# Kernel tuning notes

Hardware: AMD Instinct MI355X
Metric: run time of the kernel (lower is better)

Reference implementation:

```python
import jax, jax.numpy as jnp
import numpy as np

B, IN, CB, HD, EXP, OUT, FC1 = 512, 512, 8, 256, 128, 512, 1024
CH = CB * HD            # 2048, combiner output channels
CC = IN + CH            # 2560, concat feature size
EPS = 1e-5

def _lrelu(x):
    return jnp.where(x >= 0, x, 0.2 * x)

def _bn2(x, g, b):  # BatchNorm1d on (B, C): stats over batch
    m = x.mean(0)
    v = x.var(0)
    return (x - m) * jax.lax.rsqrt(v + EPS) * g + b

def _bn3(x, g, b):  # BatchNorm1d/2d on (B, C, L): stats over (batch, length)
    m = x.mean((0, 2), keepdims=True)
    v = x.var((0, 2), keepdims=True)
    return (x - m) * jax.lax.rsqrt(v + EPS) * g[None, :, None] + b[None, :, None]

def _cmix(W, x):  # 1x1 conv over channels: (O,I) x (B,I,L) -> (B,O,L)
    return jnp.einsum('oi,bil->bol', W, x)

def setup_inputs() -> dict:
    key = jax.random.key(0)
    ks = jax.random.split(key, 16)
    def w(k, o, i):
        return jax.random.normal(k, (o, i), jnp.float32) * (1.0 / np.sqrt(i))
    u = jax.random.uniform(ks[1], (B, CB, HD, 1), jnp.float32, 1e-6, 1.0 - 1e-6)
    return {
        'x': jax.random.normal(ks[0], (B, IN), jnp.float32),
        'gumbel': -jnp.log(-jnp.log(u)),
        # combiner (Linear no-bias + BN + LeakyReLU) x3
        'cW1': w(ks[2], 2 * IN, IN), 'cg1': jnp.ones(2 * IN), 'cb1': jnp.zeros(2 * IN),
        'cW2': w(ks[3], 2 * IN, 2 * IN), 'cg2': jnp.ones(2 * IN), 'cb2': jnp.zeros(2 * IN),
        'cW3': w(ks[4], CH, 2 * IN), 'cg3': jnp.ones(CH), 'cb3': jnp.zeros(CH),
        # encoder Conv2d1x1 stack 1 -> 32 -> 64 -> 128
        'eW1': w(ks[5], EXP // 4, 1), 'eg1': jnp.ones(EXP // 4), 'eb1': jnp.zeros(EXP // 4),
        'eW2': w(ks[6], EXP // 2, EXP // 4), 'eg2': jnp.ones(EXP // 2), 'eb2': jnp.zeros(EXP // 2),
        'eW3': w(ks[7], EXP, EXP // 2), 'eg3': jnp.ones(EXP), 'eb3': jnp.zeros(EXP),
        # fc Conv1d1x1: 2560 -> 1024 (BN+lrelu), 1024 -> OUT (bias, no act)
        'fW1': w(ks[8], FC1, CC), 'fg1': jnp.ones(FC1), 'fb1': jnp.zeros(FC1),
        'fW2': w(ks[9], OUT, FC1), 'fbias2': jnp.zeros(OUT),
        # decoder Conv1d1x1: 128 -> 64 -> 32 -> 1
        'dW1': w(ks[10], EXP // 2, EXP), 'dg1': jnp.ones(EXP // 2), 'db1': jnp.zeros(EXP // 2),
        'dW2': w(ks[11], EXP // 4, EXP // 2), 'dg2': jnp.ones(EXP // 4), 'db2': jnp.zeros(EXP // 4),
        'dW3': w(ks[12], 1, EXP // 4), 'dbias3': jnp.zeros(1),
    }

def _forward(x, gumbel, cW1, cg1, cb1, cW2, cg2, cb2, cW3, cg3, cb3,
             eW1, eg1, eb1, eW2, eg2, eb2, eW3, eg3, eb3,
             fW1, fg1, fb1, fW2, fbias2,
             dW1, dg1, db1, dW2, dg2, db2, dW3, dbias3):
    # ---- combiner: logits for gumbel-softmax hard codebook selection ----
    h = _lrelu(_bn2(x @ cW1.T, cg1, cb1))
    h = _lrelu(_bn2(h @ cW2.T, cg2, cb2))
    logits = _lrelu(_bn2(h @ cW3.T, cg3, cb3)).reshape(B, CB, HD, 1)
    y = jax.nn.softmax(logits + gumbel, axis=1)  # tau = 1 (torch default)
    hard = jax.nn.one_hot(jnp.argmax(y, axis=1), CB, axis=1, dtype=y.dtype)
    w = (hard - jax.lax.stop_gradient(y) + y)[..., 0]  # (B, CB, HD) straight-through
    # weight last dim is size-1, so broadcast-mul + sum(-1) against x collapses
    # exactly to w * sum_j x_j (same math, no (B,CB,HD,IN) intermediate).
    S = x.sum(-1)          # (B,)
    S2 = (x * x).sum(-1)   # (B,)
    xs = (w * S[:, None, None]).reshape(B, CH)
    xp = (w * S2[:, None, None]).reshape(B, CH)
    z = (xs * xs - xp) * 0.5
    feat = jnp.concatenate([x, z], axis=-1)  # (B, CC)
    # ---- encoder: Conv2d1x1 stack on (B,1,1,CC) == channel mix over length CC ----
    t = feat[:, None, :]  # (B, 1, CC)
    t = _lrelu(_bn3(_cmix(eW1, t), eg1, eb1))
    t = _lrelu(_bn3(_cmix(eW2, t), eg2, eb2))
    t = _lrelu(_bn3(_cmix(eW3, t), eg3, eb3))  # (B, EXP, CC)
    # ---- fc: Conv1d over channels=CC, length=EXP ----
    t = jnp.swapaxes(t, 1, 2)  # (B, CC, EXP)
    t = _lrelu(_bn3(_cmix(fW1, t), fg1, fb1))          # (B, FC1, EXP)
    t = _cmix(fW2, t) + fbias2[None, :, None]          # (B, OUT, EXP)
    # ---- decoder: Conv1d over channels=EXP, length=OUT ----
    t = jnp.swapaxes(t, 1, 2)  # (B, EXP, OUT)
    t = _lrelu(_bn3(_cmix(dW1, t), dg1, db1))
    t = _lrelu(_bn3(_cmix(dW2, t), dg2, db2))
    t = _cmix(dW3, t) + dbias3[None, :, None]  # (B, 1, OUT)
    return t[:, 0, :]  # (B, OUT)

def reference(x, gumbel, cW1, cg1, cb1, cW2, cg2, cb2, cW3, cg3, cb3,
              eW1, eg1, eb1, eW2, eg2, eb2, eW3, eg3, eb3,
              fW1, fg1, fb1, fW2, fbias2,
              dW1, dg1, db1, dW2, dg2, db2, dW3, dbias3):
    return _forward(x, gumbel, cW1, cg1, cb1, cW2, cg2, cb2, cW3, cg3, cb3,
                    eW1, eg1, eb1, eW2, eg2, eb2, eW3, eg3, eb3,
                    fW1, fg1, fb1, fW2, fbias2,
                    dW1, dg1, db1, dW2, dg2, db2, dW3, dbias3)
```

## Files before the change

kernel.cpp:

```cpp
#include <hip/hip_runtime.h>
#include <cstddef>

#define DEV __device__ __forceinline__
DEV float lrelu(float x){ return x >= 0.0f ? x : 0.2f*x; }
typedef _Float16 f16;
typedef _Float16 f16x8 __attribute__((ext_vector_type(8)));
typedef float f32x4 __attribute__((ext_vector_type(4)));

DEV f16x8 splat8(f16 s){ f16x8 v = {s,s,s,s,s,s,s,s}; return v; }
DEV f16x8 bnl8(f16x8 v, f16x8 sc, f16x8 sh){
    f16x8 t = v*sc + sh;
    f16x8 z = splat8((f16)0.0f);
    f16x8 mx = __builtin_elementwise_max(t, z);
    f16x8 mn = __builtin_elementwise_min(t, z);
    return mx + mn*splat8((f16)0.2f);
}

DEV void gload_lds16(const f16* src, f16* dst){
    __builtin_amdgcn_global_load_lds(
        (const __attribute__((address_space(1))) void*)src,
        (__attribute__((address_space(3))) void*)dst, 16, 0, 0);
}

DEV void dma_pair(const f16* g0, const f16* g1, f16* ldsbase, int t){
    gload_lds16(g0, ldsbase + t*8);
    gload_lds16(g1, ldsbase + 2048 + t*8);
}
DEV int swz_off(int r, int g){ return r*32 + ((g ^ ((r>>1)&3))<<3); }

#define SCHED0 __builtin_amdgcn_sched_barrier(0)
#define BARRIER __builtin_amdgcn_s_barrier()

constexpr int NXPT = 512*512;

constexpr size_t O_H1  = 0;
constexpr size_t O_H2  = O_H1 + 512*1024;
constexpr size_t O_L   = O_H2 + 512*1024;
constexpr size_t O_SEL = O_L  + 512*2048;
constexpr size_t O_S   = O_SEL + 512*256;
constexpr size_t O_S2  = O_S + 512;
constexpr size_t O_VAL = O_S2 + 512;
constexpr size_t O_PRM = O_VAL + 512;
constexpr size_t P_SC1=0, P_SH1=1024, P_SC2=2048, P_SH2=3072, P_SC3=4096, P_SH3=6144;
constexpr size_t P_A1=8192, P_C1=8224, P_EW2T=8256 ;
constexpr size_t P_ACC2=18496 , P_ACC3=18624 ;
constexpr size_t P_SCE2=18880, P_SHE2=18944, P_SCE3=19008, P_SHE3=19136;
constexpr size_t P_U0=19264 , P_FTOT=19392 ;
constexpr size_t P_SCF1=20416, P_SHF1=21440;
constexpr size_t P_SCD1=22464, P_SHD1=22528, P_SCD2=22592, P_SHD2=22624;
constexpr size_t P_SCE3H=22656, P_SHE3H=22720;
constexpr size_t P_SCF1H=22784, P_SHF1H=23296;
constexpr size_t P_SCE2H=23808, P_SHE2H=23840;
constexpr size_t PRM_SIZE = 32768;
constexpr size_t O_PF  = O_H1;
constexpr size_t O_PD1 = O_H2;
constexpr size_t O_PD2 = O_H2 + 262144;
constexpr size_t O_FW1H = O_L;
constexpr size_t O_FW2H = O_L + 262144;
constexpr size_t O_ACCF = O_L + 524288;
constexpr size_t O_DW1H = O_L + 528384;
constexpr size_t O_EW3H = O_L + 532480;
constexpr size_t O_V2SS = O_L + 536576;
constexpr size_t O_U1  = O_PRM + PRM_SIZE;
constexpr size_t O_P1  = O_U1 + 512*128;
constexpr size_t O_FZT = O_P1 + 512*1024;
constexpr size_t O_V3S = O_FZT + (size_t)2048*1024;
constexpr size_t O_BIG1= O_V3S + 513*128;
constexpr size_t O_BIG2= O_BIG1 + (size_t)512*512*128/2;
constexpr size_t O_D1  = O_BIG2;
constexpr size_t O_D2  = O_BIG2 + (size_t)512*64*512;
constexpr size_t O_END = O_BIG2 + (size_t)512*1024*128/2;

#define FMA44(av,bv) do{ \
  acc[0][0]=fmaf(av.x,bv.x,acc[0][0]); acc[0][1]=fmaf(av.x,bv.y,acc[0][1]); \
  acc[0][2]=fmaf(av.x,bv.z,acc[0][2]); acc[0][3]=fmaf(av.x,bv.w,acc[0][3]); \
  acc[1][0]=fmaf(av.y,bv.x,acc[1][0]); acc[1][1]=fmaf(av.y,bv.y,acc[1][1]); \
  acc[1][2]=fmaf(av.y,bv.z,acc[1][2]); acc[1][3]=fmaf(av.y,bv.w,acc[1][3]); \
  acc[2][0]=fmaf(av.z,bv.x,acc[2][0]); acc[2][1]=fmaf(av.z,bv.y,acc[2][1]); \
  acc[2][2]=fmaf(av.z,bv.z,acc[2][2]); acc[2][3]=fmaf(av.z,bv.w,acc[2][3]); \
  acc[3][0]=fmaf(av.w,bv.x,acc[3][0]); acc[3][1]=fmaf(av.w,bv.y,acc[3][1]); \
  acc[3][2]=fmaf(av.w,bv.z,acc[3][2]); acc[3][3]=fmaf(av.w,bv.w,acc[3][3]); \
}while(0)

__global__ void k_sentinel(float* out){ out[blockIdx.x*256 + threadIdx.x] = 1.0e6f; }

__global__ __launch_bounds__(256) void k_prep(
    const float* __restrict__ fW1, const float* __restrict__ fW2,
    const float* __restrict__ dW1, const float* __restrict__ eW3,
    f16* __restrict__ fW1h, f16* __restrict__ fW2h, f16* __restrict__ dW1h,
    f16* __restrict__ eW3h, float* __restrict__ accAll)
{
    const int i = blockIdx.x*256 + threadIdx.x;
    int f = i >> 9, l = i & 511;
    fW1h[i] = (f16)fW1[(size_t)f*2560 + l];
    fW2h[i] = (f16)fW2[i];
    if (i < 8192) { dW1h[i] = (f16)dW1[i]; eW3h[i] = (f16)eW3[i]; }
    if (i < 4096) accAll[i] = 0.f;
}

__global__ __launch_bounds__(256) void k_gemm_c(
    const float* __restrict__ A, const float* __restrict__ W, float* __restrict__ C,
    int N, int K, const float* __restrict__ sc, const float* __restrict__ sh)
{
    __shared__ __align__(16) float As[16][68];
    __shared__ __align__(16) float Ws[16][68];
    const int n0 = blockIdx.x * 64, m0 = blockIdx.y * 64;
    const int t = threadIdx.x;
    const int kk = t & 15, ri = t >> 4;
    const int tx = t & 15, ty = t >> 4;
    float acc[4][4] = {{0.f,0.f,0.f,0.f},{0.f,0.f,0.f,0.f},{0.f,0.f,0.f,0.f},{0.f,0.f,0.f,0.f}};
    for (int k0 = 0; k0 < K; k0 += 16) {
        float scv = 0.f, shv = 0.f;
        if (sc) { scv = sc[k0+kk]; shv = sh[k0+kk]; }
        #pragma unroll
        for (int mm = 0; mm < 4; ++mm) {
            float v = A[(size_t)(m0 + ri + mm*16) * K + k0 + kk];
            if (sc) v = lrelu(fmaf(v, scv, shv));
            As[kk][ri + mm*16] = v;
        }
        #pragma unroll
        for (int nn = 0; nn < 4; ++nn)
            Ws[kk][ri + nn*16] = W[(size_t)(n0 + ri + nn*16) * K + k0 + kk];
        __syncthreads();
        #pragma unroll
        for (int kq = 0; kq < 16; ++kq) {
            const float4 av = *reinterpret_cast<const float4*>(&As[kq][ty*4]);
            const float4 bv = *reinterpret_cast<const float4*>(&Ws[kq][tx*4]);
            FMA44(av, bv);
        }
        __syncthreads();
    }
    #pragma unroll
    for (int i = 0; i < 4; ++i)
        #pragma unroll
        for (int j = 0; j < 4; ++j)
            C[(size_t)(m0 + ty*4 + i) * N + n0 + tx*4 + j] = acc[i][j];
}

__global__ __launch_bounds__(256) void k_stats2d_p(
    const float* __restrict__ buf, int C, float* __restrict__ part)
{
    const int t = threadIdx.x;
    const int r0 = blockIdx.x*16;
    const int c0 = blockIdx.y*1024;
    float s[4]={0.f,0.f,0.f,0.f}, s2[4]={0.f,0.f,0.f,0.f};
    for (int rr = 0; rr < 16; ++rr) {
        float4 v = *reinterpret_cast<const float4*>(buf + (size_t)(r0+rr)*C + c0 + t*4);
        s[0]+=v.x; s[1]+=v.y; s[2]+=v.z; s[3]+=v.w;
        s2[0]+=v.x*v.x; s2[1]+=v.y*v.y; s2[2]+=v.z*v.z; s2[3]+=v.w*v.w;
    }
    float* d0 = part + (size_t)blockIdx.x*2*C + c0 + t*4;
    *reinterpret_cast<float4*>(d0)     = (float4){s[0],s[1],s[2],s[3]};
    *reinterpret_cast<float4*>(d0 + C) = (float4){s2[0],s2[1],s2[2],s2[3]};
}

__global__ __launch_bounds__(256) void k_sel(
    const float* __restrict__ Lpre, const float* __restrict__ gumbel,
    const float* __restrict__ sc, const float* __restrict__ sh, int* __restrict__ sel)
{
    const int b = blockIdx.x, hd = threadIdx.x;
    float best = -3.0e38f; int bi = 0;
    #pragma unroll
    for (int cb = 0; cb < 8; ++cb) {
        int c = cb*256 + hd;
        float v = lrelu(fmaf(Lpre[(size_t)b*2048 + c], sc[c], sh[c])) + gumbel[(size_t)b*2048 + c];
        if (v > best) { best = v; bi = cb; }
    }
    sel[b*256 + hd] = bi;
}

__global__ __launch_bounds__(256) void k_val(const float* __restrict__ x,
    float* __restrict__ S, float* __restrict__ S2, float* __restrict__ val)
{
    const int b = blockIdx.x, t = threadIdx.x;
    float v0 = x[b*512 + t], v1 = x[b*512 + t + 256];
    __shared__ float ls[256], ls2[256];
    ls[t] = v0 + v1; ls2[t] = v0*v0 + v1*v1;
    __syncthreads();
    for (int off = 128; off; off >>= 1) { if (t < off) { ls[t]+=ls[t+off]; ls2[t]+=ls2[t+off]; } __syncthreads(); }
    if (t == 0) { float s = ls[0], s2 = ls2[0]; S[b]=s; S2[b]=s2; val[b]=0.5f*(s*s - s2); }
}

__global__ __launch_bounds__(256) void k_e1params(
    const float* __restrict__ S, const float* __restrict__ S2, const float* __restrict__ val,
    const float* __restrict__ eW1, const float* __restrict__ eg1, const float* __restrict__ eb1,
    float* __restrict__ A1, float* __restrict__ C1, float* __restrict__ accs )
{
    const int t = threadIdx.x;
    accs[t] = 0.f; if (t < 128) accs[256 + t] = 0.f;
    __shared__ float ls[256], ls2[256];
    float s = 0.f, s2 = 0.f;
    for (int b = t; b < 512; b += 256) {
        float vb = val[b];
        s  += S[b]  + 256.f*vb;
        s2 += S2[b] + 256.f*vb*vb;
    }
    ls[t] = s; ls2[t] = s2; __syncthreads();
    for (int off = 128; off; off >>= 1) { if (t < off) { ls[t]+=ls[t+off]; ls2[t]+=ls2[t+off]; } __syncthreads(); }
    if (t < 32) {
        const float invn = 1.0f/1310720.f;
        float mu = ls[0]*invn;
        float var = fmaxf(ls2[0]*invn - mu*mu, 0.f);
        float w = eW1[t];
        float rs = 1.0f / sqrtf(w*w*var + 1e-5f);
        float a = w * eg1[t] * rs;
        A1[t] = a; C1[t] = eb1[t] - mu*a;
    }
}

__global__ void k_wtrans2(const float* __restrict__ eW2, float* __restrict__ eW2T)
{
    const int t = threadIdx.x;
    for (int i = t; i < 2048; i += 256) { int p = i >> 5, o = i & 31; eW2T[o*64 + p] = eW2[i]; }
}

__global__ __launch_bounds__(256) void k_transpose_fz(const float* __restrict__ fW1, float* __restrict__ fzT)
{
    __shared__ float tile[64][65];
    const int z0 = blockIdx.x*64, f0 = blockIdx.y*64;
    const int j = threadIdx.x & 63, i0 = threadIdx.x >> 6;
    #pragma unroll
    for (int ii = 0; ii < 16; ++ii) {
        int fi = i0*16 + ii;
        tile[fi][j] = fW1[(size_t)(f0+fi)*2560 + 512 + z0 + j];
    }
    __syncthreads();
    #pragma unroll
    for (int ii = 0; ii < 16; ++ii) {
        int zi = i0*16 + ii;
        fzT[(size_t)(z0+zi)*1024 + f0 + j] = tile[j][zi];
    }
}

__global__ __launch_bounds__(256) void k_ftot(const float* __restrict__ fzT, float* __restrict__ Ftot)
{
    const int f = blockIdx.x*256 + threadIdx.x;
    float s = 0.f;
    for (int z = 0; z < 2048; ++z) s += fzT[(size_t)z*1024 + f];
    Ftot[f] = s;
}

__global__ __launch_bounds__(256) void k_p1(const float* __restrict__ fzT, const int* __restrict__ sel,
                                            float* __restrict__ P1)
{
    const int b = blockIdx.x, t = threadIdx.x;
    float a0=0.f, a1=0.f, a2=0.f, a3=0.f;
    for (int hd = 0; hd < 256; ++hd) {
        int col = sel[b*256 + hd]*256 + hd;
        const float* r = fzT + (size_t)col*1024;
        a0 += r[t]; a1 += r[t+256]; a2 += r[t+512]; a3 += r[t+768];
    }
    P1[b*1024 + t] = a0; P1[b*1024 + t + 256] = a1; P1[b*1024 + t + 512] = a2; P1[b*1024 + t + 768] = a3;
}

__global__ __launch_bounds__(256) void k_epass2(
    const float* __restrict__ x,
    const float* __restrict__ A1, const float* __restrict__ C1,
    const float* __restrict__ eW2T, f16* __restrict__ V2x)
{
    __shared__ float sW[2048], sA[32], sC[32];
    const int t = threadIdx.x;
    #pragma unroll
    for (int i = 0; i < 8; ++i) sW[t + 256*i] = eW2T[t + 256*i];
    if (t < 32) { sA[t] = A1[t]; sC[t] = C1[t]; }
    __syncthreads();
    const int pt = blockIdx.x*256 + t;
    float phi = x[pt];
    float v2[64];
    #pragma unroll
    for (int p = 0; p < 64; ++p) v2[p] = 0.f;
    for (int o = 0; o < 32; ++o) {
        float t1 = lrelu(fmaf(sA[o], phi, sC[o]));
        #pragma unroll
        for (int p = 0; p < 64; ++p) v2[p] = fmaf(sW[o*64 + p], t1, v2[p]);
    }
    f16* dst = V2x + (size_t)pt*64;
    #pragma unroll
    for (int dd = 0; dd < 64; dd += 8) {
        f16x8 o;
        #pragma unroll
        for (int e = 0; e < 8; ++e) o[e] = (f16)v2[dd+e];
        *reinterpret_cast<f16x8*>(dst + dd) = o;
    }
}

__global__ __launch_bounds__(64) void k_esupport2(
    const float* __restrict__ val,
    const float* __restrict__ A1, const float* __restrict__ C1,
    const float* __restrict__ eW2T, float* __restrict__ V2s)
{
    const int idx = blockIdx.x, d = threadIdx.x;
    float phi = (idx < 512) ? val[idx] : 0.f;
    __shared__ float t1s[32];
    if (d < 32) t1s[d] = lrelu(fmaf(A1[d], phi, C1[d]));
    __syncthreads();
    float s = 0.f;
    #pragma unroll
    for (int o = 0; o < 32; ++o) s = fmaf(eW2T[o*64 + d], t1s[o], s);
    V2s[idx*64 + d] = s;
}

__global__ __launch_bounds__(64) void k_wstats(
    const float* __restrict__ V, int C, float* __restrict__ acc)
{
    const int c = blockIdx.x, lane = threadIdx.x;
    float s = 0.f, s2 = 0.f;
    for (int i = lane; i < 513; i += 64) {
        float w = (i < 512) ? 256.f : 917504.f;
        float v = V[(size_t)i*C + c];
        s += w*v; s2 += w*v*v;
    }
    #pragma unroll
    for (int off = 32; off; off >>= 1) { s += __shfl_xor(s, off); s2 += __shfl_xor(s2, off); }
    if (lane == 0) { atomicAdd(&acc[c], s); atomicAdd(&acc[C + c], s2); }
}

__global__ __launch_bounds__(256) void k_stats_v2scan(const f16* __restrict__ V2x, float* __restrict__ acc2)
{
    const int t = threadIdx.x;
    const int wave = t >> 6, lane = t & 63;
    const int g = t & 7;
    const int slot = blockIdx.x*32 + (t >> 3);
    float s[8] = {0,0,0,0,0,0,0,0}, s2[8] = {0,0,0,0,0,0,0,0};
    for (int p = slot; p < NXPT; p += 2048) {
        f16x8 v = *reinterpret_cast<const f16x8*>(V2x + (size_t)p*64 + g*8);
        #pragma unroll
        for (int e = 0; e < 8; ++e) { float f = (float)v[e]; s[e] += f; s2[e] += f*f; }
    }
    #pragma unroll
    for (int off = 8; off <= 32; off <<= 1) {
        #pragma unroll
        for (int e = 0; e < 8; ++e) { s[e] += __shfl_xor(s[e], off); s2[e] += __shfl_xor(s2[e], off); }
    }
    __shared__ float red[4*128];
    if (lane < 8) {
        #pragma unroll
        for (int e = 0; e < 8; ++e) {
            red[wave*128 + lane*16 + e]     = s[e];
            red[wave*128 + lane*16 + 8 + e] = s2[e];
        }
    }
    __syncthreads();
    if (t < 128) {
        float v = red[t] + red[128 + t] + red[256 + t] + red[384 + t];
        int gg = t >> 4, k = t & 15;
        if (k < 8) atomicAdd(&acc2[gg*8 + k], v);
        else       atomicAdd(&acc2[64 + gg*8 + (k - 8)], v);
    }
}

__global__ void k_finalize(const float* __restrict__ acc, int C, float invn,
                           const float* __restrict__ g, const float* __restrict__ bb,
                           float* __restrict__ sc, float* __restrict__ sh,
                           f16* __restrict__ sch, f16* __restrict__ shh)
{
    const int idx = blockIdx.x*blockDim.x + threadIdx.x;
    if (idx < C) {
        float m = acc[idx] * invn;
        float var = fmaxf(acc[C + idx] * invn - m*m, 0.f);
        float r = 1.0f / sqrtf(var + 1e-5f);
        float s = g[idx] * r;
        float h = bb[idx] - m*s;
        sc[idx] = s; sh[idx] = h;
        if (sch) { sch[idx] = (f16)s; shh[idx] = (f16)h; }
    }
}

__global__ void k_finalize_p(const float* __restrict__ P, int C, int nPart, float invn,
                             const float* __restrict__ g, const float* __restrict__ bb,
                             float* __restrict__ sc, float* __restrict__ sh,
                             f16* __restrict__ sch, f16* __restrict__ shh)
{
    const int idx = blockIdx.x*blockDim.x + threadIdx.x;
    if (idx < C) {
        float s = 0.f, s2 = 0.f;
        for (int p = 0; p < nPart; ++p) {
            s  += P[(size_t)p*2*C + idx];
            s2 += P[(size_t)p*2*C + C + idx];
        }
        float m = s * invn;
        float var = fmaxf(s2 * invn - m*m, 0.f);
        float r = 1.0f / sqrtf(var + 1e-5f);
        float sv = g[idx] * r;
        float h = bb[idx] - m*sv;
        sc[idx] = sv; sh[idx] = h;
        if (sch) { sch[idx] = (f16)sv; shh[idx] = (f16)h; }
    }
}

__global__ __launch_bounds__(256) void k_finalize_e3(
    const float* __restrict__ P, const float* __restrict__ accw,
    const float* __restrict__ g, const float* __restrict__ bb,
    float* __restrict__ sc, float* __restrict__ sh,
    f16* __restrict__ sch, f16* __restrict__ shh)
{
    const int t = threadIdx.x, q = t & 127, h = t >> 7;
    float s = 0.f, s2 = 0.f;
    for (int p = h*1024; p < h*1024 + 1024; ++p) {
        s  += P[(size_t)p*256 + q];
        s2 += P[(size_t)p*256 + 128 + q];
    }
    __shared__ float red[2][2][128];
    red[h][0][q] = s; red[h][1][q] = s2;
    __syncthreads();
    if (t < 128) {
        float ss  = red[0][0][q] + red[1][0][q] + accw[q];
        float ss2 = red[0][1][q] + red[1][1][q] + accw[128 + q];
        const float invn = 1.0f/1310720.f;
        float m = ss * invn;
        float var = fmaxf(ss2 * invn - m*m, 0.f);
        float r = 1.0f / sqrtf(var + 1e-5f);
        float sv = g[q] * r, hh = bb[q] - m*sv;
        sc[q] = sv; sh[q] = hh; sch[q] = (f16)sv; shh[q] = (f16)hh;
    }
}

__global__ __launch_bounds__(256) void k_finalize_f(
    const float* __restrict__ P,
    const float* __restrict__ g, const float* __restrict__ bb,
    float* __restrict__ sc, float* __restrict__ sh,
    f16* __restrict__ sch, f16* __restrict__ shh)
{
    const int f = blockIdx.x*256 + threadIdx.x;
    const int fb = f >> 7, c = f & 127;
    const float* base = P + (size_t)fb*512*256 + c;
    float s = 0.f, s2 = 0.f;
    for (int b = 0; b < 512; ++b) {
        s  += base[(size_t)b*256];
        s2 += base[(size_t)b*256 + 128];
    }
    float m = s*(1.0f/65536.f);
    float var = fmaxf(s2*(1.0f/65536.f) - m*m, 0.f);
    float r = 1.0f/sqrtf(var + 1e-5f);
    float sv = g[f]*r, h = bb[f] - m*sv;
    sc[f] = sv; sh[f] = h; sch[f] = (f16)sv; shh[f] = (f16)h;
}

__global__ __launch_bounds__(256) void k_finalize_d1(
    const float* __restrict__ P,
    const float* __restrict__ g, const float* __restrict__ bb,
    float* __restrict__ sc, float* __restrict__ sh)
{
    const int t = threadIdx.x, d = t & 63, gr = t >> 6;
    float s = 0.f, s2 = 0.f;
    for (int p = gr*512; p < gr*512 + 512; ++p) {
        s  += P[(size_t)p*128 + d];
        s2 += P[(size_t)p*128 + 64 + d];
    }
    __shared__ float red[4][2][64];
    red[gr][0][d] = s; red[gr][1][d] = s2;
    __syncthreads();
    if (t < 64) {
        float ss  = red[0][0][t]+red[1][0][t]+red[2][0][t]+red[3][0][t];
        float ss2 = red[0][1][t]+red[1][1][t]+red[2][1][t]+red[3][1][t];
        float m = ss*(1.0f/262144.f);
        float var = fmaxf(ss2*(1.0f/262144.f) - m*m, 0.f);
        float r = 1.0f/sqrtf(var + 1e-5f);
        float sv = g[t]*r;
        sc[t] = sv; sh[t] = bb[t] - m*sv;
    }
}

__global__ __launch_bounds__(256) void k_finalize_d2(
    const float* __restrict__ P,
    const float* __restrict__ g, const float* __restrict__ bb,
    float* __restrict__ sc, float* __restrict__ sh)
{
    const int t = threadIdx.x, e = t & 31, gr = t >> 5;
    float s = 0.f, s2 = 0.f;
    for (int p = gr*512; p < gr*512 + 512; ++p) {
        s  += P[(size_t)p*64 + e];
        s2 += P[(size_t)p*64 + 32 + e];
    }
    __shared__ float red[8][2][32];
    red[gr][0][e] = s; red[gr][1][e] = s2;
    __syncthreads();
    if (t < 32) {
        float ss = 0.f, ss2 = 0.f;
        #pragma unroll
        for (int k2 = 0; k2 < 8; ++k2) { ss += red[k2][0][t]; ss2 += red[k2][1][t]; }
        float m = ss*(1.0f/262144.f);
        float var = fmaxf(ss2*(1.0f/262144.f) - m*m, 0.f);
        float r = 1.0f/sqrtf(var + 1e-5f);
        float sv = g[t]*r;
        sc[t] = sv; sh[t] = bb[t] - m*sv;
    }
}

__global__ __launch_bounds__(256) void k_mfma_e3(
    const f16* __restrict__ eW3h, const f16* __restrict__ V2x,
    const f16* __restrict__ sc2h, const f16* __restrict__ sh2h,
    f16* __restrict__ V3xT, float* __restrict__ pE3)
{
    __shared__ __align__(16) f16 As[128][76];
    __shared__ __align__(16) f16 Bs[128][76];
    __shared__ float rede[256];
    const int b = blockIdx.y, l0 = blockIdx.x * 128;
    const int t = threadIdx.x;
    const int wave = t >> 6, lane = t & 63;
    const int quad = lane >> 4, l16 = lane & 15;
    const int row = t >> 1, half = t & 1;
    #pragma unroll
    for (int c = 0; c < 4; ++c)
        *reinterpret_cast<f16x8*>(&As[row][half*32 + c*8]) =
            *reinterpret_cast<const f16x8*>(eW3h + row*64 + half*32 + c*8);
    const f16* src = V2x + ((size_t)(b*512 + l0 + row))*64 + half*32;
    #pragma unroll
    for (int c = 0; c < 4; ++c) {
        f16x8 v = *reinterpret_cast<const f16x8*>(src + c*8);
        const f16x8 csc = *reinterpret_cast<const f16x8*>(sc2h + half*32 + c*8);
        const f16x8 csh = *reinterpret_cast<const f16x8*>(sh2h + half*32 + c*8);
        *reinterpret_cast<f16x8*>(&Bs[row][half*32 + c*8]) = bnl8(v, csc, csh);
    }
    __syncthreads();
    f32x4 acc[2][8];
    #pragma unroll
    for (int i = 0; i < 2; ++i)
        #pragma unroll
        for (int j = 0; j < 8; ++j) acc[i][j] = (f32x4){0.f,0.f,0.f,0.f};
    f16x8 a0  = *reinterpret_cast<const f16x8*>(&As[32*wave + l16][quad*8]);
    f16x8 a0b = *reinterpret_cast<const f16x8*>(&As[32*wave + l16][32 + quad*8]);
    f16x8 a1  = *reinterpret_cast<const f16x8*>(&As[32*wave + 16 + l16][quad*8]);
    f16x8 a1b = *reinterpret_cast<const f16x8*>(&As[32*wave + 16 + l16][32 + quad*8]);
    #pragma unroll
    for (int j = 0; j < 8; ++j) {
        f16x8 bj  = *reinterpret_cast<const f16x8*>(&Bs[16*j + l16][quad*8]);
        f16x8 bjb = *reinterpret_cast<const f16x8*>(&Bs[16*j + l16][32 + quad*8]);
        acc[0][j] = __builtin_amdgcn_mfma_f32_16x16x32_f16(a0,  bj,  acc[0][j], 0, 0, 0);
        acc[0][j] = __builtin_amdgcn_mfma_f32_16x16x32_f16(a0b, bjb, acc[0][j], 0, 0, 0);
        acc[1][j] = __builtin_amdgcn_mfma_f32_16x16x32_f16(a1,  bj,  acc[1][j], 0, 0, 0);
        acc[1][j] = __builtin_amdgcn_mfma_f32_16x16x32_f16(a1b, bjb, acc[1][j], 0, 0, 0);
    }
    float se[8] = {0,0,0,0,0,0,0,0}, s2e[8] = {0,0,0,0,0,0,0,0};
    #pragma unroll
    for (int i = 0; i < 2; ++i) {
        #pragma unroll
        for (int r = 0; r < 4; ++r) {
            int q = 32*wave + 16*i + quad*4 + r;
            #pragma unroll
            for (int j = 0; j < 8; ++j) {
                float v = acc[i][j][r];
                V3xT[((size_t)b*128 + q)*512 + l0 + 16*j + l16] = (f16)v;
                se[i*4+r] += v; s2e[i*4+r] += v*v;
            }
        }
    }
    #pragma unroll
    for (int k = 0; k < 8; ++k) {
        se[k]  += __shfl_xor(se[k],1);  se[k]  += __shfl_xor(se[k],2);
        se[k]  += __shfl_xor(se[k],4);  se[k]  += __shfl_xor(se[k],8);
        s2e[k] += __shfl_xor(s2e[k],1); s2e[k] += __shfl_xor(s2e[k],2);
        s2e[k] += __shfl_xor(s2e[k],4); s2e[k] += __shfl_xor(s2e[k],8);
    }
    if (l16 == 0) {
        #pragma unroll
        for (int i = 0; i < 2; ++i)
            #pragma unroll
            for (int r = 0; r < 4; ++r) {
                int qq = 32*wave + 16*i + quad*4 + r;
                rede[qq] = se[i*4+r];
            }
    }
    __syncthreads();
    if (t < 128) pE3[((size_t)(blockIdx.x*512 + b))*256 + t] = rede[t];
    __syncthreads();
    if (l16 == 0) {
        #pragma unroll
        for (int i = 0; i < 2; ++i)
            #pragma unroll
            for (int r = 0; r < 4; ++r) {
                int qq = 32*wave + 16*i + quad*4 + r;
                rede[qq] = s2e[i*4+r];
            }
    }
    __syncthreads();
    if (t < 128) pE3[((size_t)(blockIdx.x*512 + b))*256 + 128 + t] = rede[t];
}

__global__ __launch_bounds__(128) void k_esupport3(
    const float* __restrict__ V2s, const float* __restrict__ sc2, const float* __restrict__ sh2,
    const float* __restrict__ eW3, float* __restrict__ V3s)
{
    const int idx = blockIdx.x, q = threadIdx.x;
    __shared__ float t2s[64];
    if (q < 64) t2s[q] = lrelu(fmaf(sc2[q], V2s[idx*64 + q], sh2[q]));
    __syncthreads();
    float s = 0.f;
    #pragma unroll
    for (int d = 0; d < 64; ++d) s = fmaf(eW3[q*64 + d], t2s[d], s);
    V3s[idx*128 + q] = s;
}

__global__ void k_u(const float* __restrict__ V3s, const float* __restrict__ sc3, const float* __restrict__ sh3,
                    float* __restrict__ u1, float* __restrict__ u0)
{
    const int idx = blockIdx.x*256 + threadIdx.x;
    if (idx < 513*128) {
        int i = idx >> 7, q = idx & 127;
        float tv = lrelu(fmaf(sc3[q], V3s[idx], sh3[q]));
        if (i < 512) u1[idx] = tv; else u0[q] = tv;
    }
}

__global__ __launch_bounds__(256) void k_mfma_fw1T(
    const f16* __restrict__ fW1h, const f16* __restrict__ V3xT,
    const f16* __restrict__ sceh, const f16* __restrict__ sheh,
    const float* __restrict__ u1, const float* __restrict__ u0,
    const float* __restrict__ P1, const float* __restrict__ Ftot,
    f16* __restrict__ out6T, float* __restrict__ pF)
{
    __shared__ __align__(16) f16 lds[24576];
    __shared__ float redf[1024];
    const int t = threadIdx.x;
    const int wave = t >> 6, lane = t & 63;
    const int quad = lane >> 4, l16 = lane & 15;
    const int n = blockIdx.x + (blockIdx.y << 3);
    const int b = (n & 7)*64 + (n >> 6);
    const int fblk = (n >> 3) & 7;
    const int f0 = fblk * 128;
    const f16* Aa = V3xT + (size_t)b*65536;
    const f16* Bb = fW1h + (size_t)f0*512;
    const int sg = (t & 3) ^ ((t >> 3) & 3);
    const size_t go0 = (size_t)(t >> 2)*512 + sg*8;
    const size_t go1 = go0 + (size_t)64*512;
    const int rA0 = 32*wave + l16, rA1 = rA0 + 16;
    const f16x8 scA0 = splat8(sceh[rA0]), shA0 = splat8(sheh[rA0]);
    const f16x8 scA1 = splat8(sceh[rA1]), shA1 = splat8(sheh[rA1]);
    const int offA0 = swz_off(rA0, quad);
    const int offA1 = swz_off(rA1, quad);
    int offB[8];
    #pragma unroll
    for (int j = 0; j < 8; ++j) offB[j] = swz_off(16*j + l16, quad);
    float p1j[8], p0j[8], u1q[8], u0q[8];
    #pragma unroll
    for (int j = 0; j < 8; ++j) {
        int f = f0 + 16*j + l16;
        p1j[j] = P1[b*1024 + f];
        p0j[j] = Ftot[f] - p1j[j];
    }
    #pragma unroll
    for (int i = 0; i < 2; ++i)
        #pragma unroll
        for (int r = 0; r < 4; ++r) {
            int q = 32*wave + 16*i + quad*4 + r;
            u1q[i*4+r] = u1[b*128 + q];
            u0q[i*4+r] = u0[q];
        }
    f32x4 acc[2][8];
    #pragma unroll
    for (int i = 0; i < 2; ++i)
        #pragma unroll
        for (int j = 0; j < 8; ++j) acc[i][j] = (f32x4){0.f,0.f,0.f,0.f};
    dma_pair(Aa + go0,      Aa + go1,      lds,               t);
    dma_pair(Bb + go0,      Bb + go1,      lds + 4096,        t);
    dma_pair(Aa + 32 + go0, Aa + 32 + go1, lds + 8192,        t);
    dma_pair(Bb + 32 + go0, Bb + 32 + go1, lds + 8192 + 4096, t);
    int m = 0;
    for (int kt = 0; kt < 16; ++kt) {
        SCHED0; BARRIER; SCHED0;
        if (kt <= 13) {
            const int mp = (m >= 1) ? m - 1 : m + 2;
            const int k0 = (kt + 2) * 32;
            dma_pair(Aa + k0 + go0, Aa + k0 + go1, lds + mp*8192,        t);
            dma_pair(Bb + k0 + go0, Bb + k0 + go1, lds + mp*8192 + 4096, t);
            asm volatile("s_waitcnt vmcnt(8)" ::: "memory");
        } else if (kt == 14) {
            asm volatile("s_waitcnt vmcnt(4)" ::: "memory");
        } else {
            asm volatile("s_waitcnt vmcnt(0)" ::: "memory");
        }
        SCHED0; BARRIER; SCHED0;
        const f16* As = lds + m*8192;
        const f16* Bs = As + 4096;
        f16x8 a0 = bnl8(*reinterpret_cast<const f16x8*>(As + offA0), scA0, shA0);
        f16x8 a1 = bnl8(*reinterpret_cast<const f16x8*>(As + offA1), scA1, shA1);
        #pragma unroll
        for (int j = 0; j < 8; ++j) {
            f16x8 bj = *reinterpret_cast<const f16x8*>(Bs + offB[j]);
            acc[0][j] = __builtin_amdgcn_mfma_f32_16x16x32_f16(a0, bj, acc[0][j], 0, 0, 0);
            acc[1][j] = __builtin_amdgcn_mfma_f32_16x16x32_f16(a1, bj, acc[1][j], 0, 0, 0);
        }
        m = (m == 2) ? 0 : m + 1;
    }
    float sj[8], s2j[8];
    #pragma unroll
    for (int j = 0; j < 8; ++j) { sj[j] = 0.f; s2j[j] = 0.f; }
    #pragma unroll
    for (int i = 0; i < 2; ++i) {
        #pragma unroll
        for (int r = 0; r < 4; ++r) {
            int q = 32*wave + 16*i + quad*4 + r;
            #pragma unroll
            for (int j = 0; j < 8; ++j) {
                int f = f0 + 16*j + l16;
                float v = acc[i][j][r] + u1q[i*4+r]*p1j[j] + u0q[i*4+r]*p0j[j];
                out6T[((size_t)b*128 + q)*1024 + f] = (f16)v;
                sj[j] += v; s2j[j] += v*v;
            }
        }
    }
    #pragma unroll
    for (int j = 0; j < 8; ++j) {
        sj[j]  += __shfl_xor(sj[j],16);  sj[j]  += __shfl_xor(sj[j],32);
        s2j[j] += __shfl_xor(s2j[j],16); s2j[j] += __shfl_xor(s2j[j],32);
    }
    if (quad == 0) {
        #pragma unroll
        for (int j = 0; j < 8; ++j) {
            redf[wave*256 + j*16 + l16]       = sj[j];
            redf[wave*256 + 128 + j*16 + l16] = s2j[j];
        }
    }
    __syncthreads();
    {
        float v = redf[t] + redf[256 + t] + redf[512 + t] + redf[768 + t];
        pF[((size_t)(fblk*512 + b))*256 + t] = v;
    }
}

__global__ __launch_bounds__(256) void k_mfma_fw2T(
    const f16* __restrict__ fW2h, const f16* __restrict__ out6T,
    const f16* __restrict__ scfh, const f16* __restrict__ shfh,
    const float* __restrict__ fbias2, f16* __restrict__ out7)
{
    __shared__ __align__(16) f16 lds[24576];
    __shared__ __align__(16) f16 scL[1024];
    __shared__ __align__(16) f16 shL[1024];
    const int t = threadIdx.x;
    const int wave = t >> 6, lane = t & 63;
    const int quad = lane >> 4, l16 = lane & 15;
    const int n = blockIdx.x + (blockIdx.y << 2);
    const int b = (n & 7)*64 + (n >> 5);
    const int o0 = ((n >> 3) & 3) * 128;
    const f16* Aa = fW2h + (size_t)o0*1024;
    const f16* Bb = out6T + (size_t)b*131072;
    const int sg = (t & 3) ^ ((t >> 3) & 3);
    const size_t go0 = (size_t)(t >> 2)*1024 + sg*8;
    const size_t go1 = go0 + (size_t)64*1024;
    const int bnO = sg*8;
    const int offA0 = swz_off(32*wave + l16, quad);
    const int offA1 = swz_off(32*wave + 16 + l16, quad);
    int offB[8];
    #pragma unroll
    for (int j = 0; j < 8; ++j) offB[j] = swz_off(16*j + l16, quad);
    float biasv[8];
    #pragma unroll
    for (int i = 0; i < 2; ++i)
        #pragma unroll
        for (int r = 0; r < 4; ++r)
            biasv[i*4+r] = fbias2[o0 + 32*wave + 16*i + quad*4 + r];
    f32x4 acc[2][8];
    #pragma unroll
    for (int i = 0; i < 2; ++i)
        #pragma unroll
        for (int j = 0; j < 8; ++j) acc[i][j] = (f32x4){0.f,0.f,0.f,0.f};
    if (t < 128) *reinterpret_cast<f16x8*>(&scL[t*8]) =
        *reinterpret_cast<const f16x8*>(scfh + t*8);
    else         *reinterpret_cast<f16x8*>(&shL[(t-128)*8]) =
        *reinterpret_cast<const f16x8*>(shfh + (t-128)*8);
    __syncthreads();
    dma_pair(Aa + go0,      Aa + go1,      lds,               t);
    dma_pair(Bb + go0,      Bb + go1,      lds + 4096,        t);
    dma_pair(Aa + 32 + go0, Aa + 32 + go1, lds + 8192,        t);
    dma_pair(Bb + 32 + go0, Bb + 32 + go1, lds + 8192 + 4096, t);
    int m = 0;
    for (int kt = 0; kt < 32; ++kt) {
        SCHED0; BARRIER; SCHED0;
        if (kt <= 29) {
            const int mp = (m >= 1) ? m - 1 : m + 2;
            const int k0 = (kt + 2) * 32;
            dma_pair(Aa + k0 + go0, Aa + k0 + go1, lds + mp*8192,        t);
            dma_pair(Bb + k0 + go0, Bb + k0 + go1, lds + mp*8192 + 4096, t);
            asm volatile("s_waitcnt vmcnt(8)" ::: "memory");
        } else if (kt == 30) {
            asm volatile("s_waitcnt vmcnt(4)" ::: "memory");
        } else {
            asm volatile("s_waitcnt vmcnt(0)" ::: "memory");
        }
        SCHED0; BARRIER; SCHED0;
        {
            f16* Bm = lds + m*8192 + 4096;
            const f16x8 csc = *reinterpret_cast<const f16x8*>(&scL[kt*32 + bnO]);
            const f16x8 csh = *reinterpret_cast<const f16x8*>(&shL[kt*32 + bnO]);
            f16x8 v0 = *reinterpret_cast<const f16x8*>(Bm + t*8);
            f16x8 v1 = *reinterpret_cast<const f16x8*>(Bm + 2048 + t*8);
            *reinterpret_cast<f16x8*>(Bm + t*8)        = bnl8(v0, csc, csh);
            *reinterpret_cast<f16x8*>(Bm + 2048 + t*8) = bnl8(v1, csc, csh);
        }
        asm volatile("s_waitcnt lgkmcnt(0)" ::: "memory");
        SCHED0; BARRIER; SCHED0;
        const f16* As = lds + m*8192;
        const f16* Bs = As + 4096;
        f16x8 a0 = *reinterpret_cast<const f16x8*>(As + offA0);
        f16x8 a1 = *reinterpret_cast<const f16x8*>(As + offA1);
        #pragma unroll
        for (int j = 0; j < 8; ++j) {
            f16x8 bj = *reinterpret_cast<const f16x8*>(Bs + offB[j]);
            acc[0][j] = __builtin_amdgcn_mfma_f32_16x16x32_f16(a0, bj, acc[0][j], 0, 0, 0);
            acc[1][j] = __builtin_amdgcn_mfma_f32_16x16x32_f16(a1, bj, acc[1][j], 0, 0, 0);
        }
        m = (m == 2) ? 0 : m + 1;
    }
    #pragma unroll
    for (int i = 0; i < 2; ++i) {
        #pragma unroll
        for (int r = 0; r < 4; ++r) {
            int o = o0 + 32*wave + 16*i + quad*4 + r;
            #pragma unroll
            for (int j = 0; j < 8; ++j) {
                int q = 16*j + l16;
                out7[((size_t)b*512 + o)*128 + q] = (f16)(acc[i][j][r] + biasv[i*4+r]);
            }
        }
    }
}

__global__ __launch_bounds__(256) void k_mfma_d1(
    const f16* __restrict__ dW1h, const f16* __restrict__ out7,
    f16* __restrict__ d1pre, float* __restrict__ pD1)
{
    __shared__ __align__(16) f16 As[64][44];
    __shared__ __align__(16) f16 Bs[128][44];
    __shared__ float redd[128];
    const int b = blockIdx.y, o0 = blockIdx.x * 128;
    const int t = threadIdx.x;
    const int wave = t >> 6, lane = t & 63;
    const int quad = lane >> 4, l16 = lane & 15;
    const int row0 = t >> 2, grp = t & 3;
    const f16* Bb = out7 + (size_t)b*65536;
    f32x4 acc[8];
    #pragma unroll
    for (int j = 0; j < 8; ++j) acc[j] = (f32x4){0.f,0.f,0.f,0.f};
    for (int k0 = 0; k0 < 128; k0 += 32) {
        *reinterpret_cast<f16x8*>(&As[row0][grp*8]) =
            *reinterpret_cast<const f16x8*>(dW1h + row0*128 + k0 + grp*8);
        #pragma unroll
        for (int p = 0; p < 2; ++p) {
            const int row = row0 + 64*p;
            *reinterpret_cast<f16x8*>(&Bs[row][grp*8]) =
                *reinterpret_cast<const f16x8*>(Bb + (size_t)(o0+row)*128 + k0 + grp*8);
        }
        __syncthreads();
        f16x8 a0 = *reinterpret_cast<const f16x8*>(&As[16*wave + l16][quad*8]);
        #pragma unroll
        for (int j = 0; j < 8; ++j) {
            f16x8 bj = *reinterpret_cast<const f16x8*>(&Bs[16*j + l16][quad*8]);
            acc[j] = __builtin_amdgcn_mfma_f32_16x16x32_f16(a0, bj, acc[j], 0, 0, 0);
        }
        __syncthreads();
    }
    float sd[4] = {0,0,0,0}, s2d[4] = {0,0,0,0};
    #pragma unroll
    for (int r = 0; r < 4; ++r) {
        int d = 16*wave + quad*4 + r;
        #pragma unroll
        for (int j = 0; j < 8; ++j) {
            int o = o0 + 16*j + l16;
            float v = acc[j][r];
            d1pre[(size_t)b*32768 + (size_t)d*512 + o] = (f16)v;
            sd[r] += v; s2d[r] += v*v;
        }
    }
    #pragma unroll
    for (int r = 0; r < 4; ++r) {
        sd[r]  += __shfl_xor(sd[r],1);  sd[r]  += __shfl_xor(sd[r],2);
        sd[r]  += __shfl_xor(sd[r],4);  sd[r]  += __shfl_xor(sd[r],8);
        s2d[r] += __shfl_xor(s2d[r],1); s2d[r] += __shfl_xor(s2d[r],2);
        s2d[r] += __shfl_xor(s2d[r],4); s2d[r] += __shfl_xor(s2d[r],8);
    }
    if (l16 == 0) {
        #pragma unroll
        for (int r = 0; r < 4; ++r) {
            int dd = 16*wave + quad*4 + r;
            redd[dd] = sd[r]; redd[64 + dd] = s2d[r];
        }
    }
    __syncthreads();
    if (t < 128) pD1[((size_t)(blockIdx.x*512 + b))*128 + t] = redd[t];
}

__global__ __launch_bounds__(128) void k_gemm_d2(
    const float* __restrict__ dW2, const f16* __restrict__ d1pre,
    const float* __restrict__ scd, const float* __restrict__ shd,
    float* __restrict__ d2pre, float* __restrict__ pD2)
{
    __shared__ __align__(16) float As[16][36];
    __shared__ __align__(16) float Bs[16][68];
    __shared__ float sred[64];
    const int n0 = blockIdx.x * 64, b = blockIdx.y;
    const int t = threadIdx.x;
    const int kk = t & 15, ri = t >> 4;
    const int qv = t & 63, kh = t >> 6;
    const int tx = t & 15, ty = t >> 4;
    float acc[4][4] = {{0.f,0.f,0.f,0.f},{0.f,0.f,0.f,0.f},{0.f,0.f,0.f,0.f},{0.f,0.f,0.f,0.f}};
    for (int k0 = 0; k0 < 64; k0 += 16) {
        #pragma unroll
        for (int mm = 0; mm < 4; ++mm)
            As[kk][ri + mm*8] = dW2[(ri + mm*8)*64 + k0 + kk];
        #pragma unroll
        for (int ki = 0; ki < 8; ++ki) {
            int d = k0 + kh + ki*2;
            float v = (float)d1pre[(size_t)b*32768 + (size_t)d*512 + n0 + qv];
            Bs[kh + ki*2][qv] = lrelu(fmaf(scd[d], v, shd[d]));
        }
        __syncthreads();
        #pragma unroll
        for (int kq = 0; kq < 16; ++kq) {
            const float4 av = *reinterpret_cast<const float4*>(&As[kq][ty*4]);
            const float4 bv = *reinterpret_cast<const float4*>(&Bs[kq][tx*4]);
            FMA44(av, bv);
        }
        __syncthreads();
    }
    #pragma unroll
    for (int i = 0; i < 4; ++i) {
        float s = 0.f, s2 = 0.f;
        #pragma unroll
        for (int j = 0; j < 4; ++j) {
            float v = acc[i][j];
            d2pre[(size_t)b*16384 + (size_t)(ty*4 + i)*512 + n0 + tx*4 + j] = v;
            s += v; s2 += v*v;
        }
        s  += __shfl_xor(s,1);  s  += __shfl_xor(s,2);
        s  += __shfl_xor(s,4);  s  += __shfl_xor(s,8);
        s2 += __shfl_xor(s2,1); s2 += __shfl_xor(s2,2);
        s2 += __shfl_xor(s2,4); s2 += __shfl_xor(s2,8);
        if (tx == 0) {
            int e = ty*4 + i;
            sred[e] = s; sred[32 + e] = s2;
        }
    }
    __syncthreads();
    if (t < 64) pD2[((size_t)(blockIdx.y*8 + blockIdx.x))*64 + t] = sred[t];
}

__global__ __launch_bounds__(256) void k_d3(
    const float* __restrict__ d2pre, const float* __restrict__ dW3,
    const float* __restrict__ sce, const float* __restrict__ she,
    const float* __restrict__ dbias3, float* __restrict__ out)
{
    const int idx = blockIdx.x*256 + threadIdx.x;
    const int b = idx >> 9, o = idx & 511;
    float s = dbias3[0];
    for (int e = 0; e < 32; ++e) {
        float v = d2pre[(size_t)b*16384 + e*512 + o];
        s = fmaf(dW3[e], lrelu(fmaf(v, sce[e], she[e])), s);
    }
    out[idx] = s;
}

extern "C" void kernel_launch(void* const* d_in, const int* in_sizes, int n_in,
                              void* d_out, int out_size, void* d_ws, size_t ws_size,
                              hipStream_t stream)
{
    (void)in_sizes; (void)n_in; (void)out_size;
    const float* x      = (const float*)d_in[0];
    const float* gumbel = (const float*)d_in[1];
    const float* cW1 = (const float*)d_in[2];
    const float* cg1 = (const float*)d_in[3];
    const float* cb1 = (const float*)d_in[4];
    const float* cW2 = (const float*)d_in[5];
    const float* cg2 = (const float*)d_in[6];
    const float* cb2 = (const float*)d_in[7];
    const float* cW3 = (const float*)d_in[8];
    const float* cg3 = (const float*)d_in[9];
    const float* cb3 = (const float*)d_in[10];
    const float* eW1 = (const float*)d_in[11];
    const float* eg1 = (const float*)d_in[12];
    const float* eb1 = (const float*)d_in[13];
    const float* eW2 = (const float*)d_in[14];
    const float* eg2 = (const float*)d_in[15];
    const float* eb2 = (const float*)d_in[16];
    const float* eW3 = (const float*)d_in[17];
    const float* eg3 = (const float*)d_in[18];
    const float* eb3 = (const float*)d_in[19];
    const float* fW1 = (const float*)d_in[20];
    const float* fg1 = (const float*)d_in[21];
    const float* fb1 = (const float*)d_in[22];
    const float* fW2 = (const float*)d_in[23];
    const float* fbias2 = (const float*)d_in[24];
    const float* dW1 = (const float*)d_in[25];
    const float* dg1 = (const float*)d_in[26];
    const float* db1 = (const float*)d_in[27];
    const float* dW2 = (const float*)d_in[28];
    const float* dg2 = (const float*)d_in[29];
    const float* db2 = (const float*)d_in[30];
    const float* dW3 = (const float*)d_in[31];
    const float* dbias3 = (const float*)d_in[32];
    float* out = (float*)d_out;
    float* ws  = (float*)d_ws;

    if (ws_size < O_END * sizeof(float)) {
        k_sentinel<<<1024,256,0,stream>>>(out);
        return;
    }

    float* H1  = ws + O_H1;
    float* H2  = ws + O_H2;
    float* L   = ws + O_L;
    int*   sel = (int*)(ws + O_SEL);
    float* S   = ws + O_S;
    float* S2  = ws + O_S2;
    float* val = ws + O_VAL;
    float* prm = ws + O_PRM;
    f16*   fW1h= (f16*)(ws + O_FW1H);
    f16*   fW2h= (f16*)(ws + O_FW2H);
    float* accF= ws + O_ACCF;
    f16*   dW1h= (f16*)(ws + O_DW1H);
    f16*   eW3h= (f16*)(ws + O_EW3H);
    float* V2s = ws + O_V2SS;
    float* u1  = ws + O_U1;
    float* P1  = ws + O_P1;
    float* fzT = ws + O_FZT;
    float* V3s = ws + O_V3S;
    float* pF  = ws + O_PF;
    float* pD1 = ws + O_PD1;
    float* pD2 = ws + O_PD2;
    float* p2d = ws + O_P1;
    float* pE3 = ws + O_FZT;
    f16*   V3xT= (f16*)(ws + O_BIG1);
    f16*   out7= (f16*)(ws + O_BIG1);
    f16*   out6T=(f16*)(ws + O_BIG2);
    f16*   V2x = (f16*)(ws + O_BIG2);
    f16*   d1p = (f16*)(ws + O_D1);
    float* d2p = ws + O_D2;

    const float invN_e = 1.0f/1310720.f;

    k_gemm_c<<<dim3(16,8),256,0,stream>>>(x,  cW1, H1, 1024, 512,  nullptr,     nullptr);
    k_stats2d_p<<<dim3(32,1),256,0,stream>>>(H1, 1024, p2d);
    k_finalize_p<<<4,256,0,stream>>>(p2d, 1024, 32, 1.0f/512.f, cg1, cb1,
                                     prm+P_SC1, prm+P_SH1, nullptr, nullptr);
    k_gemm_c<<<dim3(16,8),256,0,stream>>>(H1, cW2, H2, 1024, 1024, prm+P_SC1, prm+P_SH1);
    k_stats2d_p<<<dim3(32,1),256,0,stream>>>(H2, 1024, p2d);
    k_finalize_p<<<4,256,0,stream>>>(p2d, 1024, 32, 1.0f/512.f, cg2, cb2,
                                     prm+P_SC2, prm+P_SH2, nullptr, nullptr);
    k_gemm_c<<<dim3(32,8),256,0,stream>>>(H2, cW3, L,  2048, 1024, prm+P_SC2, prm+P_SH2);
    k_stats2d_p<<<dim3(32,2),256,0,stream>>>(L, 2048, p2d);
    k_finalize_p<<<8,256,0,stream>>>(p2d, 2048, 32, 1.0f/512.f, cg3, cb3,
                                     prm+P_SC3, prm+P_SH3, nullptr, nullptr);
    k_sel<<<512,256,0,stream>>>(L, gumbel, prm+P_SC3, prm+P_SH3, sel);

    k_prep<<<2048,256,0,stream>>>(fW1, fW2, dW1, eW3, fW1h, fW2h, dW1h, eW3h, accF);
    k_val<<<512,256,0,stream>>>(x, S, S2, val);
    k_e1params<<<1,256,0,stream>>>(S, S2, val, eW1, eg1, eb1, prm+P_A1, prm+P_C1, prm+P_ACC2);
    k_transpose_fz<<<dim3(32,16),256,0,stream>>>(fW1, fzT);
    k_wtrans2<<<1,256,0,stream>>>(eW2, prm+P_EW2T);
    k_ftot<<<4,256,0,stream>>>(fzT, prm+P_FTOT);
    k_p1<<<512,256,0,stream>>>(fzT, sel, P1);

    k_epass2<<<1024,256,0,stream>>>(x, prm+P_A1, prm+P_C1, prm+P_EW2T, V2x);
    k_esupport2<<<513,64,0,stream>>>(val, prm+P_A1, prm+P_C1, prm+P_EW2T, V2s);
    k_stats_v2scan<<<64,256,0,stream>>>(V2x, prm+P_ACC2);
    k_wstats<<<64,64,0,stream>>>(V2s, 64, prm+P_ACC2);
    k_finalize<<<1,256,0,stream>>>(prm+P_ACC2, 64, invN_e, eg2, eb2, prm+P_SCE2, prm+P_SHE2,
                                   (f16*)(prm+P_SCE2H), (f16*)(prm+P_SHE2H));
    k_mfma_e3<<<dim3(4,512),256,0,stream>>>(eW3h, V2x,
                                            (const f16*)(prm+P_SCE2H), (const f16*)(prm+P_SHE2H),
                                            V3xT, pE3);
    k_esupport3<<<513,128,0,stream>>>(V2s, prm+P_SCE2, prm+P_SHE2, eW3, V3s);
    k_wstats<<<128,64,0,stream>>>(V3s, 128, prm+P_ACC3);
    k_finalize_e3<<<1,256,0,stream>>>(pE3, prm+P_ACC3, eg3, eb3, prm+P_SCE3, prm+P_SHE3,
                                      (f16*)(prm+P_SCE3H), (f16*)(prm+P_SHE3H));
    k_u<<<257,256,0,stream>>>(V3s, prm+P_SCE3, prm+P_SHE3, u1, prm+P_U0);

    k_mfma_fw1T<<<dim3(8,512),256,0,stream>>>(fW1h, V3xT,
                                              (const f16*)(prm+P_SCE3H), (const f16*)(prm+P_SHE3H),
                                              u1, prm+P_U0, P1, prm+P_FTOT, out6T, pF);
    k_finalize_f<<<4,256,0,stream>>>(pF, fg1, fb1, prm+P_SCF1, prm+P_SHF1,
                                     (f16*)(prm+P_SCF1H), (f16*)(prm+P_SHF1H));
    k_mfma_fw2T<<<dim3(4,512),256,0,stream>>>(fW2h, out6T,
                                              (const f16*)(prm+P_SCF1H), (const f16*)(prm+P_SHF1H),
                                              fbias2, out7);

    k_mfma_d1<<<dim3(4,512),256,0,stream>>>(dW1h, out7, d1p, pD1);
    k_finalize_d1<<<1,256,0,stream>>>(pD1, dg1, db1, prm+P_SCD1, prm+P_SHD1);
    k_gemm_d2<<<dim3(8,512),128,0,stream>>>(dW2, d1p, prm+P_SCD1, prm+P_SHD1, d2p, pD2);
    k_finalize_d2<<<1,256,0,stream>>>(pD2, dg2, db2, prm+P_SCD2, prm+P_SHD2);
    k_d3<<<1024,256,0,stream>>>(d2p, dW3, prm+P_SCD2, prm+P_SHD2, dbias3, out);
}
```

Measured before the change: 924.3 us.

## Split Ftot column sum, merge e3 stat writes, store d2pre as fp16

Splits the serial 2048-row column reduction for Ftot (previously only 4 blocks) into 64 partial-sum blocks plus a small finishing kernel, to expose more parallelism. Merges the two LDS staging passes in k_mfma_e3's stat output into one, removing two barriers. Stores the d2 intermediate in fp16 instead of fp32 to halve its write and read traffic, at some precision cost. The partial buffer reuses the H1 workspace region, which is assumed to be free at that point.

```diff
diff --git a/kernel.cpp b/kernel.cpp
--- a/kernel.cpp
+++ b/kernel.cpp
@@ -232,11 +232,20 @@
     }
 }
 
-__global__ __launch_bounds__(256) void k_ftot(const float* __restrict__ fzT, float* __restrict__ Ftot)
+__global__ __launch_bounds__(256) void k_ftot_p(const float* __restrict__ fzT, float* __restrict__ part)
+{
+    const int f = blockIdx.x*256 + threadIdx.x;
+    const int z0 = blockIdx.y*128;
+    float s = 0.f;
+    for (int z = z0; z < z0 + 128; ++z) s += fzT[(size_t)z*1024 + f];
+    part[(size_t)blockIdx.y*1024 + f] = s;
+}
+__global__ __launch_bounds__(256) void k_ftot_s(const float* __restrict__ part, float* __restrict__ Ftot)
 {
     const int f = blockIdx.x*256 + threadIdx.x;
     float s = 0.f;
-    for (int z = 0; z < 2048; ++z) s += fzT[(size_t)z*1024 + f];
+    #pragma unroll
+    for (int zc = 0; zc < 16; ++zc) s += part[(size_t)zc*1024 + f];
     Ftot[f] = s;
 }
 
@@ -558,23 +567,12 @@
             #pragma unroll
             for (int r = 0; r < 4; ++r) {
                 int qq = 32*wave + 16*i + quad*4 + r;
-                rede[qq] = se[i*4+r];
+                rede[qq]       = se[i*4+r];
+                rede[128 + qq] = s2e[i*4+r];
             }
     }
     __syncthreads();
-    if (t < 128) pE3[((size_t)(blockIdx.x*512 + b))*256 + t] = rede[t];
-    __syncthreads();
-    if (l16 == 0) {
-        #pragma unroll
-        for (int i = 0; i < 2; ++i)
-            #pragma unroll
-            for (int r = 0; r < 4; ++r) {
-                int qq = 32*wave + 16*i + quad*4 + r;
-                rede[qq] = s2e[i*4+r];
-            }
-    }
-    __syncthreads();
-    if (t < 128) pE3[((size_t)(blockIdx.x*512 + b))*256 + 128 + t] = rede[t];
+    pE3[((size_t)(blockIdx.x*512 + b))*256 + t] = rede[t];
 }
 
 __global__ __launch_bounds__(128) void k_esupport3(
@@ -882,7 +880,7 @@
 __global__ __launch_bounds__(128) void k_gemm_d2(
     const float* __restrict__ dW2, const f16* __restrict__ d1pre,
     const float* __restrict__ scd, const float* __restrict__ shd,
-    float* __restrict__ d2pre, float* __restrict__ pD2)
+    f16* __restrict__ d2pre, float* __restrict__ pD2)
 {
     __shared__ __align__(16) float As[16][36];
     __shared__ __align__(16) float Bs[16][68];
@@ -918,7 +916,7 @@
         #pragma unroll
         for (int j = 0; j < 4; ++j) {
             float v = acc[i][j];
-            d2pre[(size_t)b*16384 + (size_t)(ty*4 + i)*512 + n0 + tx*4 + j] = v;
+            d2pre[(size_t)b*16384 + (size_t)(ty*4 + i)*512 + n0 + tx*4 + j] = (f16)v;
             s += v; s2 += v*v;
         }
         s  += __shfl_xor(s,1);  s  += __shfl_xor(s,2);
@@ -935,7 +933,7 @@
 }
 
 __global__ __launch_bounds__(256) void k_d3(
-    const float* __restrict__ d2pre, const float* __restrict__ dW3,
+    const f16* __restrict__ d2pre, const float* __restrict__ dW3,
     const float* __restrict__ sce, const float* __restrict__ she,
     const float* __restrict__ dbias3, float* __restrict__ out)
 {
@@ -943,7 +941,7 @@
     const int b = idx >> 9, o = idx & 511;
     float s = dbias3[0];
     for (int e = 0; e < 32; ++e) {
-        float v = d2pre[(size_t)b*16384 + e*512 + o];
+        float v = (float)d2pre[(size_t)b*16384 + e*512 + o];
         s = fmaf(dW3[e], lrelu(fmaf(v, sce[e], she[e])), s);
     }
     out[idx] = s;
@@ -1014,6 +1012,7 @@
     float* fzT = ws + O_FZT;
     float* V3s = ws + O_V3S;
     float* pF  = ws + O_PF;
+    float* pFT = ws + O_H1;
     float* pD1 = ws + O_PD1;
     float* pD2 = ws + O_PD2;
     float* p2d = ws + O_P1;
@@ -1023,7 +1022,7 @@
     f16*   out6T=(f16*)(ws + O_BIG2);
     f16*   V2x = (f16*)(ws + O_BIG2);
     f16*   d1p = (f16*)(ws + O_D1);
-    float* d2p = ws + O_D2;
+    f16*   d2p = (f16*)(ws + O_D2);
 
     const float invN_e = 1.0f/1310720.f;
 
@@ -1046,7 +1045,8 @@
     k_e1params<<<1,256,0,stream>>>(S, S2, val, eW1, eg1, eb1, prm+P_A1, prm+P_C1, prm+P_ACC2);
     k_transpose_fz<<<dim3(32,16),256,0,stream>>>(fW1, fzT);
     k_wtrans2<<<1,256,0,stream>>>(eW2, prm+P_EW2T);
-    k_ftot<<<4,256,0,stream>>>(fzT, prm+P_FTOT);
+    k_ftot_p<<<dim3(4,16),256,0,stream>>>(fzT, pFT);
+    k_ftot_s<<<4,256,0,stream>>>(pFT, prm+P_FTOT);
     k_p1<<<512,256,0,stream>>>(fzT, sel, P1);
 
     k_epass2<<<1024,256,0,stream>>>(x, prm+P_A1, prm+P_C1, prm+P_EW2T, V2x);
```

Measured after the change: 881.0 us. -4.7%, faster.
